# Kernel tuning notes

Hardware: AMD Instinct MI355X
Metric: run time of the kernel (lower is better)

Reference implementation:

```python
import jax, jax.numpy as jnp
import numpy as np

BETA = 0.5
THR = 1.0
BN_EPS = 1e-5

@jax.custom_vjp
def spike(x):
    # heaviside fire: spk = 1[x > 0]
    return (x > 0).astype(x.dtype)

def _spike_fwd(x):
    return spike(x), x

def _spike_bwd(x, g):
    # snnTorch surrogate.atan(), alpha=2: grad = (alpha/2) / (1 + (pi/2*alpha*x)^2) = 1/(1+(pi*x)^2)
    return (g / (1.0 + (jnp.pi * x) ** 2),)

spike.defvjp(_spike_fwd, _spike_bwd)

def setup_inputs() -> dict:
    key = jax.random.key(0)
    ks = jax.random.split(key, 6)
    B, T, D, O = 512, 128, 512, 10
    data = jax.random.normal(ks[0], (B, T, D), dtype=jnp.float32)
    # deterministic Dropout(0.5) mask in {0, 2} (scaled by 1/keep_prob), time-major
    u = jax.random.uniform(ks[1], (T, B, D), dtype=jnp.float32)
    drop_mask = (u > 0.5).astype(jnp.float32) * 2.0
    W1 = jax.random.normal(ks[2], (D, D), dtype=jnp.float32) / np.sqrt(D)
    b1 = jax.random.normal(ks[3], (D,), dtype=jnp.float32) * 0.01
    gamma = jnp.ones((D,), dtype=jnp.float32)
    bn_beta = jnp.zeros((D,), dtype=jnp.float32)
    W2 = jax.random.normal(ks[4], (O, D), dtype=jnp.float32) / np.sqrt(D)
    b2 = jax.random.normal(ks[5], (O,), dtype=jnp.float32) * 0.01
    return {"data": data, "drop_mask": drop_mask, "W1": W1, "b1": b1,
            "gamma": gamma, "bn_beta": bn_beta, "W2": W2, "b2": b2}

def reference(data, drop_mask, W1, b1, gamma, bn_beta, W2, b2):
    B, T, D = data.shape
    O = W2.shape[0]
    xs = jnp.transpose(data, (1, 0, 2))  # [T, B, D] time-major

    def batchnorm(x):  # training-mode BatchNorm1d over batch dim
        mean = jnp.mean(x, axis=0)
        var = jnp.mean((x - mean) ** 2, axis=0)
        return gamma * (x - mean) * jax.lax.rsqrt(var + BN_EPS) + bn_beta

    def step(carry, inp):
        mem1, spk1, mem2, spk2 = carry
        xt, mt = inp
        cur1 = batchnorm((mt * xt) @ W1.T + b1)          # dropout -> linear -> BN
        mem1 = BETA * mem1 + cur1 - spk1 * THR           # Leaky, subtract reset
        spk1 = spike(mem1 - THR)
        cur2 = spk1 @ W2.T + b2
        mem2 = BETA * mem2 + cur2 - spk2 * THR
        spk2 = spike(mem2 - THR)
        return (mem1, spk1, mem2, spk2), spk2

    init = (jnp.zeros((B, D), data.dtype), jnp.zeros((B, D), data.dtype),
            jnp.zeros((B, O), data.dtype), jnp.zeros((B, O), data.dtype))
    _, spk_rec = jax.lax.scan(step, init, (xs, drop_mask))
    return spk_rec  # [T, B, out_size] == torch.stack(spk_rec)
```

## Files before the change

### kernel.cpp

```cpp
#include <hip/hip_runtime.h>
#include <math.h>

#define B_ 512
#define T_ 128
#define D_ 512
#define O_ 10

typedef unsigned int uint32;
typedef short bf16x8 __attribute__((ext_vector_type(8)));
typedef float f32x4 __attribute__((ext_vector_type(4)));

__device__ __forceinline__ uint32 bf16rne(float f) {
    uint32 u = __float_as_uint(f);
    return (u + 0x7FFFu + ((u >> 16) & 1u)) >> 16;
}
__device__ __forceinline__ float bf16f(uint32 h) { return __uint_as_float(h << 16); }

__global__ __launch_bounds__(256)
void presplitW_kernel(const float* __restrict__ W1, unsigned short* __restrict__ Wsp)
{
    const int idx = blockIdx.x * 256 + threadIdx.x;
    const float4 v = *(const float4*)(W1 + (size_t)idx * 4);
    float vv[4] = {v.x, v.y, v.z, v.w};
    uint32 c0[4], c1[4], c2[4];
#pragma unroll
    for (int i = 0; i < 4; ++i) {
        c0[i] = bf16rne(vv[i]);
        float r = vv[i] - bf16f(c0[i]);
        c1[i] = bf16rne(r);
        float r2 = r - bf16f(c1[i]);
        c2[i] = bf16rne(r2);
    }
    const size_t base = (size_t)idx * 4;
    uint2 w;
    w.x = c0[0] | (c0[1] << 16); w.y = c0[2] | (c0[3] << 16);
    *(uint2*)(Wsp + base) = w;
    w.x = c1[0] | (c1[1] << 16); w.y = c1[2] | (c1[3] << 16);
    *(uint2*)(Wsp + 262144 + base) = w;
    w.x = c2[0] | (c2[1] << 16); w.y = c2[2] | (c2[3] << 16);
    *(uint2*)(Wsp + 524288 + base) = w;
}

#define SPW 40
#define SPL (128*SPW)

__global__ __launch_bounds__(256)
void gemm1_kernel(const float* __restrict__ data, const float* __restrict__ drop,
                  const unsigned short* __restrict__ Wsp, const float* __restrict__ b1,
                  float* __restrict__ hbuf, double* __restrict__ pSum,
                  double* __restrict__ pSq, int t0, int Tc)
{
    __shared__ __align__(16) unsigned short As3[3 * SPL];
    __shared__ __align__(16) unsigned short Ws3[3 * SPL];

    const int tid = threadIdx.x;
    const int bid = blockIdx.x;
    const int xcd = bid & 7;
    const int rest = bid >> 3;
    const int yy = rest & 3;
    const int g = (rest >> 2) * 8 + xcd;

    const int R = g * 128;
    const int tc = R >> 9;
    const int b_base = R & 511;
    const int t = t0 + tc;
    const int d0 = yy * 128;

    const int w = tid >> 6;
    const int lane = tid & 63;
    const int wm = w & 1, wn = w >> 1;
    const int q = lane >> 4, r16 = lane & 15;

    f32x4 acc[4][4];
#pragma unroll
    for (int i = 0; i < 4; ++i)
#pragma unroll
        for (int j = 0; j < 4; ++j) acc[i][j] = (f32x4){0.f, 0.f, 0.f, 0.f};

    for (int k0 = 0; k0 < 512; k0 += 32) {
#pragma unroll
        for (int i = 0; i < 2; ++i) {
            const int p = tid + i * 256;
            const int m = p >> 2;
            const int kg = (p & 3) * 8;
            const float* dsrc = data + ((size_t)(b_base + m) * T_ + t) * D_ + k0 + kg;
            const float* msrc = drop + ((size_t)t * B_ + b_base + m) * D_ + k0 + kg;
            const float4 dv0 = *(const float4*)(dsrc);
            const float4 dv1 = *(const float4*)(dsrc + 4);
            const float4 mv0 = *(const float4*)(msrc);
            const float4 mv1 = *(const float4*)(msrc + 4);
            float vv[8] = {dv0.x*mv0.x, dv0.y*mv0.y, dv0.z*mv0.z, dv0.w*mv0.w,
                           dv1.x*mv1.x, dv1.y*mv1.y, dv1.z*mv1.z, dv1.w*mv1.w};
            uint32 u0[8], u1[8], u2[8];
#pragma unroll
            for (int e = 0; e < 8; ++e) {
                u0[e] = bf16rne(vv[e]);
                const float r = vv[e] - bf16f(u0[e]);
                u1[e] = bf16rne(r);
                const float r2 = r - bf16f(u1[e]);
                u2[e] = bf16rne(r2);
            }
            const int dst = m * SPW + kg;
            uint4 pk;
            pk.x = u0[0]|(u0[1]<<16); pk.y = u0[2]|(u0[3]<<16);
            pk.z = u0[4]|(u0[5]<<16); pk.w = u0[6]|(u0[7]<<16);
            *(uint4*)(&As3[dst]) = pk;
            pk.x = u1[0]|(u1[1]<<16); pk.y = u1[2]|(u1[3]<<16);
            pk.z = u1[4]|(u1[5]<<16); pk.w = u1[6]|(u1[7]<<16);
            *(uint4*)(&As3[SPL + dst]) = pk;
            pk.x = u2[0]|(u2[1]<<16); pk.y = u2[2]|(u2[3]<<16);
            pk.z = u2[4]|(u2[5]<<16); pk.w = u2[6]|(u2[7]<<16);
            *(uint4*)(&As3[2*SPL + dst]) = pk;
        }
#pragma unroll
        for (int i = 0; i < 6; ++i) {
            const int p = tid + i * 256;
            const int s = p >> 9;
            const int rem = p & 511;
            const int n = rem >> 2;
            const int kg = (rem & 3) * 8;
            const uint4 pk = *(const uint4*)(Wsp + (size_t)s * 262144
                                             + (size_t)(d0 + n) * 512 + k0 + kg);
            *(uint4*)(&Ws3[s * SPL + n * SPW + kg]) = pk;
        }
        __syncthreads();

        bf16x8 af[4][3], bfr[4][3];
#pragma unroll
        for (int mt = 0; mt < 4; ++mt)
#pragma unroll
            for (int s = 0; s < 3; ++s)
                af[mt][s] = *(const bf16x8*)(&As3[s*SPL + (wm*64 + mt*16 + r16)*SPW + q*8]);
#pragma unroll
        for (int nt = 0; nt < 4; ++nt)
#pragma unroll
            for (int s = 0; s < 3; ++s)
                bfr[nt][s] = *(const bf16x8*)(&Ws3[s*SPL + (wn*64 + nt*16 + r16)*SPW + q*8]);

#define PRODUCT(SA, SB)                                                          \
        {                                                                        \
            _Pragma("unroll")                                                    \
            for (int mt = 0; mt < 4; ++mt) {                                     \
                _Pragma("unroll")                                                \
                for (int nt = 0; nt < 4; ++nt)                                   \
                    acc[mt][nt] = __builtin_amdgcn_mfma_f32_16x16x32_bf16(       \
                        af[mt][SA], bfr[nt][SB], acc[mt][nt], 0, 0, 0);          \
            }                                                                    \
        }
        PRODUCT(0, 0)
        PRODUCT(0, 1)
        PRODUCT(1, 0)
        PRODUCT(1, 1)
        PRODUCT(0, 2)
        PRODUCT(2, 0)
#undef PRODUCT
        __syncthreads();
    }

    float b1c[4];
#pragma unroll
    for (int nt = 0; nt < 4; ++nt) b1c[nt] = b1[d0 + wn*64 + nt*16 + r16];

    double sd[4], sq[4];
#pragma unroll
    for (int nt = 0; nt < 4; ++nt) { sd[nt] = 0.0; sq[nt] = 0.0; }

#pragma unroll
    for (int mt = 0; mt < 4; ++mt)
#pragma unroll
        for (int r = 0; r < 4; ++r) {
            const int row = R + wm*64 + mt*16 + q*4 + r;
            float* op = hbuf + (size_t)row * D_ + d0 + wn*64 + r16;
#pragma unroll
            for (int nt = 0; nt < 4; ++nt) {
                const float hf = acc[mt][nt][r] + b1c[nt];
                op[nt*16] = hf;
                const double dh = (double)hf;
                sd[nt] += dh;
                sq[nt] = fma(dh, dh, sq[nt]);
            }
        }
#pragma unroll
    for (int nt = 0; nt < 4; ++nt) {
        sd[nt] += __shfl_xor(sd[nt], 16); sd[nt] += __shfl_xor(sd[nt], 32);
        sq[nt] += __shfl_xor(sq[nt], 16); sq[nt] += __shfl_xor(sq[nt], 32);
    }
    double* dsh = (double*)&As3[0];
    __syncthreads();
    if (q == 0) {
#pragma unroll
        for (int nt = 0; nt < 4; ++nt) {
            dsh[(w*64 + nt*16 + r16)*2 + 0] = sd[nt];
            dsh[(w*64 + nt*16 + r16)*2 + 1] = sq[nt];
        }
    }
    __syncthreads();
    if (tid < 128) {
        const int col = tid;
        const int gg = col >> 6, c = col & 63;
        const double S = dsh[((2*gg)*64 + c)*2 + 0] + dsh[((2*gg+1)*64 + c)*2 + 0];
        const double Q = dsh[((2*gg)*64 + c)*2 + 1] + dsh[((2*gg+1)*64 + c)*2 + 1];
        const int bt = b_base >> 7;
        pSum[((size_t)(bt*Tc + tc))*D_ + d0 + col] = S;
        pSq [((size_t)(bt*Tc + tc))*D_ + d0 + col] = Q;
    }
}

__global__ __launch_bounds__(256)
void finalize_kernel(const double* __restrict__ pSum, const double* __restrict__ pSq,
                     const float* __restrict__ gamma, const float* __restrict__ bn_beta,
                     float* __restrict__ scaleArr, float* __restrict__ shiftArr, int Tc)
{
    const int tc = blockIdx.x;
    const int d = blockIdx.y * 256 + threadIdx.x;
    double S = 0.0, Q = 0.0;
#pragma unroll
    for (int bt = 0; bt < 4; ++bt) {
        S += pSum[((size_t)(bt * Tc + tc)) * D_ + d];
        Q += pSq [((size_t)(bt * Tc + tc)) * D_ + d];
    }
    const double mean = S / (double)B_;
    const double var  = Q / (double)B_ - mean * mean;
    const double rs   = 1.0 / sqrt(var + 1e-5);
    const double gm   = (double)gamma[d] * rs;
    scaleArr[tc * D_ + d] = (float)gm;
    shiftArr[tc * D_ + d] = (float)((double)bn_beta[d] - gm * mean);
}

__global__ __launch_bounds__(256)
void scanA_kernel(const float* __restrict__ hbuf, const float* __restrict__ scaleArr,
                  const float* __restrict__ shiftArr, unsigned short* __restrict__ spk,
                  float* __restrict__ sMem1, float* __restrict__ sSpk1, int t0, int Tc)
{
    const int idx = blockIdx.x * 256 + threadIdx.x;
    const int b = idx >> 7;
    const int d0 = (idx & 127) * 4;

    float4 m1, s1;
    if (t0 == 0) {
        m1 = make_float4(0.f, 0.f, 0.f, 0.f);
        s1 = make_float4(0.f, 0.f, 0.f, 0.f);
    } else {
        m1 = *(const float4*)(sMem1 + (size_t)b * D_ + d0);
        s1 = *(const float4*)(sSpk1 + (size_t)b * D_ + d0);
    }

    float4 hv = *(const float4*)(hbuf + (size_t)b * D_ + d0);
    float4 sc = *(const float4*)(scaleArr + d0);
    float4 sf = *(const float4*)(shiftArr + d0);

    for (int tc = 0; tc < Tc; ++tc) {
        float4 hvN, scN, sfN;
        if (tc + 1 < Tc) {
            hvN = *(const float4*)(hbuf + ((size_t)(tc + 1) * B_ + b) * D_ + d0);
            scN = *(const float4*)(scaleArr + (tc + 1) * D_ + d0);
            sfN = *(const float4*)(shiftArr + (tc + 1) * D_ + d0);
        }
        float4 cur1;
        cur1.x = fmaf(sc.x, hv.x, sf.x);
        cur1.y = fmaf(sc.y, hv.y, sf.y);
        cur1.z = fmaf(sc.z, hv.z, sf.z);
        cur1.w = fmaf(sc.w, hv.w, sf.w);

        m1.x = fmaf(0.5f, m1.x, cur1.x) - s1.x;
        m1.y = fmaf(0.5f, m1.y, cur1.y) - s1.y;
        m1.z = fmaf(0.5f, m1.z, cur1.z) - s1.z;
        m1.w = fmaf(0.5f, m1.w, cur1.w) - s1.w;

        s1.x = ((m1.x - 1.0f) > 0.f) ? 1.f : 0.f;
        s1.y = ((m1.y - 1.0f) > 0.f) ? 1.f : 0.f;
        s1.z = ((m1.z - 1.0f) > 0.f) ? 1.f : 0.f;
        s1.w = ((m1.w - 1.0f) > 0.f) ? 1.f : 0.f;

        const uint32 ux = (s1.x == 1.f) ? 0x3F80u : 0u;
        const uint32 uy = (s1.y == 1.f) ? 0x3F80u : 0u;
        const uint32 uz = (s1.z == 1.f) ? 0x3F80u : 0u;
        const uint32 uw = (s1.w == 1.f) ? 0x3F80u : 0u;
        uint2 pk;
        pk.x = ux | (uy << 16);
        pk.y = uz | (uw << 16);
        *(uint2*)(spk + ((size_t)tc * B_ + b) * D_ + d0) = pk;

        hv = hvN; sc = scN; sf = sfN;
    }

    *(float4*)(sMem1 + (size_t)b * D_ + d0) = m1;
    *(float4*)(sSpk1 + (size_t)b * D_ + d0) = s1;
}

__global__ __launch_bounds__(256)
void gemm2_kernel(const unsigned short* __restrict__ spk, const float* __restrict__ W2,
                  const float* __restrict__ b2, float* __restrict__ cur2)
{
    const int tid = threadIdx.x;
    const int w = tid >> 6, lane = tid & 63;
    const int rowBase = blockIdx.x * 64 + w * 16;

    float w2r[O_][8];
#pragma unroll
    for (int o = 0; o < O_; ++o) {
        const float4 wa = *(const float4*)(W2 + o * D_ + lane * 8);
        const float4 wb = *(const float4*)(W2 + o * D_ + lane * 8 + 4);
        w2r[o][0] = wa.x; w2r[o][1] = wa.y; w2r[o][2] = wa.z; w2r[o][3] = wa.w;
        w2r[o][4] = wb.x; w2r[o][5] = wb.y; w2r[o][6] = wb.z; w2r[o][7] = wb.w;
    }
    float b2v[O_];
#pragma unroll
    for (int o = 0; o < O_; ++o) b2v[o] = b2[o];

    for (int rr = 0; rr < 16; ++rr) {
        const int row = rowBase + rr;
        const uint4 sv = *(const uint4*)(spk + (size_t)row * D_ + lane * 8);
        float f[8];
        f[0] = bf16f(sv.x & 0xFFFFu); f[1] = bf16f(sv.x >> 16);
        f[2] = bf16f(sv.y & 0xFFFFu); f[3] = bf16f(sv.y >> 16);
        f[4] = bf16f(sv.z & 0xFFFFu); f[5] = bf16f(sv.z >> 16);
        f[6] = bf16f(sv.w & 0xFFFFu); f[7] = bf16f(sv.w >> 16);
        float p[O_];
#pragma unroll
        for (int o = 0; o < O_; ++o) {
            float v = f[0] * w2r[o][0];
#pragma unroll
            for (int j = 1; j < 8; ++j) v = fmaf(f[j], w2r[o][j], v);
            p[o] = v;
        }
#pragma unroll
        for (int o = 0; o < O_; ++o) {
#pragma unroll
            for (int off = 32; off > 0; off >>= 1)
                p[o] += __shfl_xor(p[o], off);
        }
        float outv = 0.f;
#pragma unroll
        for (int o = 0; o < O_; ++o)
            if (lane == o) outv = p[o] + b2v[o];
        if (lane < O_)
            cur2[(size_t)row * O_ + lane] = outv;
    }
}

__global__ __launch_bounds__(256)
void scanB_kernel(const float* __restrict__ cur2, float* __restrict__ out,
                  float* __restrict__ sMem2, float* __restrict__ sSpk2, int t0, int Tc)
{
    const int idx = blockIdx.x * 256 + threadIdx.x;
    float mem2, spk2;
    if (t0 == 0) { mem2 = 0.f; spk2 = 0.f; }
    else { mem2 = sMem2[idx]; spk2 = sSpk2[idx]; }

    float v[4], vn[4];
#pragma unroll
    for (int j = 0; j < 4; ++j) v[j] = cur2[(size_t)j * (B_ * O_) + idx];

    for (int tg = 0; tg < Tc; tg += 4) {
        if (tg + 4 < Tc) {
#pragma unroll
            for (int j = 0; j < 4; ++j)
                vn[j] = cur2[(size_t)(tg + 4 + j) * (B_ * O_) + idx];
        }
#pragma unroll
        for (int j = 0; j < 4; ++j) {
            mem2 = fmaf(0.5f, mem2, v[j]) - spk2;
            spk2 = ((mem2 - 1.0f) > 0.f) ? 1.f : 0.f;
            out[(size_t)(t0 + tg + j) * (B_ * O_) + idx] = spk2;
        }
#pragma unroll
        for (int j = 0; j < 4; ++j) v[j] = vn[j];
    }
    sMem2[idx] = mem2;
    sSpk2[idx] = spk2;
}

extern "C" void kernel_launch(void* const* d_in, const int* in_sizes, int n_in,
                              void* d_out, int out_size, void* d_ws, size_t ws_size,
                              hipStream_t stream) {
    const float* data    = (const float*)d_in[0];
    const float* drop    = (const float*)d_in[1];
    const float* W1      = (const float*)d_in[2];
    const float* b1      = (const float*)d_in[3];
    const float* gamma   = (const float*)d_in[4];
    const float* bn_beta = (const float*)d_in[5];
    const float* W2      = (const float*)d_in[6];
    const float* b2      = (const float*)d_in[7];
    float* out = (float*)d_out;

    const size_t fixedBytes = 1572864  + 2*1048576  + 2*20480 ;
    const size_t perT = 1048576 + 524288 + 20480 + 4096 + 32768;
    int Tc = T_;
    while (Tc > 2 && fixedBytes + (size_t)Tc * perT > ws_size) Tc >>= 1;

    char* p = (char*)d_ws;
    double* pSum    = (double*)p; p += (size_t)4 * Tc * D_ * 8;
    double* pSq     = (double*)p; p += (size_t)4 * Tc * D_ * 8;
    float* hbuf     = (float*)p; p += (size_t)Tc * B_ * D_ * 4;
    float* scaleArr = (float*)p; p += (size_t)Tc * D_ * 4;
    float* shiftArr = (float*)p; p += (size_t)Tc * D_ * 4;
    float* sMem1    = (float*)p; p += (size_t)B_ * D_ * 4;
    float* sSpk1    = (float*)p; p += (size_t)B_ * D_ * 4;
    float* sMem2    = (float*)p; p += (size_t)B_ * O_ * 4;
    float* sSpk2    = (float*)p; p += (size_t)B_ * O_ * 4;
    float* cur2     = (float*)p; p += (size_t)Tc * B_ * O_ * 4;
    unsigned short* Wsp = (unsigned short*)p; p += (size_t)3 * D_ * D_ * 2;
    unsigned short* spk = (unsigned short*)p; p += (size_t)Tc * B_ * D_ * 2;

    presplitW_kernel<<<256, 256, 0, stream>>>(W1, Wsp);

    for (int t0 = 0; t0 < T_; t0 += Tc) {
        gemm1_kernel<<<Tc * 16, 256, 0, stream>>>(data, drop, Wsp, b1, hbuf,
                                                  pSum, pSq, t0, Tc);
        finalize_kernel<<<dim3(Tc, D_ / 256), 256, 0, stream>>>(
            pSum, pSq, gamma, bn_beta, scaleArr, shiftArr, Tc);
        scanA_kernel<<<256, 256, 0, stream>>>(hbuf, scaleArr, shiftArr, spk,
                                              sMem1, sSpk1, t0, Tc);
        gemm2_kernel<<<Tc * 8, 256, 0, stream>>>(spk, W2, b2, cur2);
        scanB_kernel<<<20, 256, 0, stream>>>(cur2, out, sMem2, sSpk2, t0, Tc);
    }
}
```

Baseline: 552.5 us.

## Prefetch GEMM1 operands into registers, repad LDS, widen scanA and gemm2 grids

In gemm1, the next k-tile's data and dropout-mask loads are issued into registers while the current tile's MFMAs run, and the W slices are loaded into registers before the LDS stores. This is meant to hide global-memory latency behind compute. The LDS row pitch shrinks from 40 to 34 halfwords, which changes the bank-conflict pattern and lowers the LDS footprint. scanA now uses one scalar element per thread across 1024 blocks instead of float4 across 256 blocks, and gemm2 uses 4 rows per wave with four times as many blocks, both to expose more parallelism at the cost of narrower memory accesses.

```diff
diff --git a/kernel.cpp b/kernel.cpp
--- a/kernel.cpp
+++ b/kernel.cpp
@@ -41,7 +41,7 @@
     *(uint2*)(Wsp + 524288 + base) = w;
 }
 
-#define SPW 40
+#define SPW 34
 #define SPL (128*SPW)
 
 __global__ __launch_bounds__(256)
@@ -71,26 +71,51 @@
     const int wm = w & 1, wn = w >> 1;
     const int q = lane >> 4, r16 = lane & 15;
 
+    const int lm = tid >> 2;
+    const int kg = (tid & 3) * 8;
+
     f32x4 acc[4][4];
 #pragma unroll
     for (int i = 0; i < 4; ++i)
 #pragma unroll
         for (int j = 0; j < 4; ++j) acc[i][j] = (f32x4){0.f, 0.f, 0.f, 0.f};
 
+    float4 pd[2][2], pm[2][2];
+
+#define LOADA(K0)                                                                \
+    {                                                                            \
+        _Pragma("unroll")                                                        \
+        for (int i = 0; i < 2; ++i) {                                            \
+            const int m = lm + i * 64;                                           \
+            const float* dsrc = data + ((size_t)(b_base + m) * T_ + t) * D_ + (K0) + kg; \
+            const float* msrc = drop + ((size_t)t * B_ + b_base + m) * D_ + (K0) + kg;   \
+            pd[i][0] = *(const float4*)(dsrc);                                   \
+            pd[i][1] = *(const float4*)(dsrc + 4);                               \
+            pm[i][0] = *(const float4*)(msrc);                                   \
+            pm[i][1] = *(const float4*)(msrc + 4);                               \
+        }                                                                        \
+    }
+
+    LOADA(0)
+
     for (int k0 = 0; k0 < 512; k0 += 32) {
+        uint4 pw[6];
+#pragma unroll
+        for (int i = 0; i < 6; ++i) {
+            const int p = tid + i * 256;
+            const int s = p >> 9;
+            const int rem = p & 511;
+            const int n = rem >> 2;
+            const int kg2 = (rem & 3) * 8;
+            pw[i] = *(const uint4*)(Wsp + (size_t)s * 262144
+                                    + (size_t)(d0 + n) * 512 + k0 + kg2);
+        }
 #pragma unroll
         for (int i = 0; i < 2; ++i) {
-            const int p = tid + i * 256;
-            const int m = p >> 2;
-            const int kg = (p & 3) * 8;
-            const float* dsrc = data + ((size_t)(b_base + m) * T_ + t) * D_ + k0 + kg;
-            const float* msrc = drop + ((size_t)t * B_ + b_base + m) * D_ + k0 + kg;
-            const float4 dv0 = *(const float4*)(dsrc);
-            const float4 dv1 = *(const float4*)(dsrc + 4);
-            const float4 mv0 = *(const float4*)(msrc);
-            const float4 mv1 = *(const float4*)(msrc + 4);
-            float vv[8] = {dv0.x*mv0.x, dv0.y*mv0.y, dv0.z*mv0.z, dv0.w*mv0.w,
-                           dv1.x*mv1.x, dv1.y*mv1.y, dv1.z*mv1.z, dv1.w*mv1.w};
+            float vv[8] = {pd[i][0].x*pm[i][0].x, pd[i][0].y*pm[i][0].y,
+                           pd[i][0].z*pm[i][0].z, pd[i][0].w*pm[i][0].w,
+                           pd[i][1].x*pm[i][1].x, pd[i][1].y*pm[i][1].y,
+                           pd[i][1].z*pm[i][1].z, pd[i][1].w*pm[i][1].w};
             uint32 u0[8], u1[8], u2[8];
 #pragma unroll
             for (int e = 0; e < 8; ++e) {
@@ -100,7 +125,7 @@
                 const float r2 = r - bf16f(u1[e]);
                 u2[e] = bf16rne(r2);
             }
-            const int dst = m * SPW + kg;
+            const int dst = (lm + i * 64) * SPW + kg;
             uint4 pk;
             pk.x = u0[0]|(u0[1]<<16); pk.y = u0[2]|(u0[3]<<16);
             pk.z = u0[4]|(u0[5]<<16); pk.w = u0[6]|(u0[7]<<16);
@@ -118,10 +143,8 @@
             const int s = p >> 9;
             const int rem = p & 511;
             const int n = rem >> 2;
-            const int kg = (rem & 3) * 8;
-            const uint4 pk = *(const uint4*)(Wsp + (size_t)s * 262144
-                                             + (size_t)(d0 + n) * 512 + k0 + kg);
-            *(uint4*)(&Ws3[s * SPL + n * SPW + kg]) = pk;
+            const int kg2 = (rem & 3) * 8;
+            *(uint4*)(&Ws3[s * SPL + n * SPW + kg2]) = pw[i];
         }
         __syncthreads();
 
@@ -136,6 +159,8 @@
 #pragma unroll
             for (int s = 0; s < 3; ++s)
                 bfr[nt][s] = *(const bf16x8*)(&Ws3[s*SPL + (wn*64 + nt*16 + r16)*SPW + q*8]);
+
+        if (k0 + 32 < 512) LOADA(k0 + 32)
 
 #define PRODUCT(SA, SB)                                                          \
         {                                                                        \
@@ -232,60 +257,35 @@
                   const float* __restrict__ shiftArr, unsigned short* __restrict__ spk,
                   float* __restrict__ sMem1, float* __restrict__ sSpk1, int t0, int Tc)
 {
-    const int idx = blockIdx.x * 256 + threadIdx.x;
-    const int b = idx >> 7;
-    const int d0 = (idx & 127) * 4;
-
-    float4 m1, s1;
-    if (t0 == 0) {
-        m1 = make_float4(0.f, 0.f, 0.f, 0.f);
-        s1 = make_float4(0.f, 0.f, 0.f, 0.f);
-    } else {
-        m1 = *(const float4*)(sMem1 + (size_t)b * D_ + d0);
-        s1 = *(const float4*)(sSpk1 + (size_t)b * D_ + d0);
-    }
-
-    float4 hv = *(const float4*)(hbuf + (size_t)b * D_ + d0);
-    float4 sc = *(const float4*)(scaleArr + d0);
-    float4 sf = *(const float4*)(shiftArr + d0);
+    const int e = blockIdx.x * 256 + threadIdx.x;
+    const int b = e >> 9;
+    const int d = e & 511;
+
+    float m1, s1;
+    if (t0 == 0) { m1 = 0.f; s1 = 0.f; }
+    else { m1 = sMem1[e]; s1 = sSpk1[e]; }
+
+    float hv = hbuf[e];
+    float sc = scaleArr[d];
+    float sf = shiftArr[d];
 
     for (int tc = 0; tc < Tc; ++tc) {
-        float4 hvN, scN, sfN;
+        float hvN, scN, sfN;
         if (tc + 1 < Tc) {
-            hvN = *(const float4*)(hbuf + ((size_t)(tc + 1) * B_ + b) * D_ + d0);
-            scN = *(const float4*)(scaleArr + (tc + 1) * D_ + d0);
-            sfN = *(const float4*)(shiftArr + (tc + 1) * D_ + d0);
-        }
-        float4 cur1;
-        cur1.x = fmaf(sc.x, hv.x, sf.x);
-        cur1.y = fmaf(sc.y, hv.y, sf.y);
-        cur1.z = fmaf(sc.z, hv.z, sf.z);
-        cur1.w = fmaf(sc.w, hv.w, sf.w);
-
-        m1.x = fmaf(0.5f, m1.x, cur1.x) - s1.x;
-        m1.y = fmaf(0.5f, m1.y, cur1.y) - s1.y;
-        m1.z = fmaf(0.5f, m1.z, cur1.z) - s1.z;
-        m1.w = fmaf(0.5f, m1.w, cur1.w) - s1.w;
-
-        s1.x = ((m1.x - 1.0f) > 0.f) ? 1.f : 0.f;
-        s1.y = ((m1.y - 1.0f) > 0.f) ? 1.f : 0.f;
-        s1.z = ((m1.z - 1.0f) > 0.f) ? 1.f : 0.f;
-        s1.w = ((m1.w - 1.0f) > 0.f) ? 1.f : 0.f;
-
-        const uint32 ux = (s1.x == 1.f) ? 0x3F80u : 0u;
-        const uint32 uy = (s1.y == 1.f) ? 0x3F80u : 0u;
-        const uint32 uz = (s1.z == 1.f) ? 0x3F80u : 0u;
-        const uint32 uw = (s1.w == 1.f) ? 0x3F80u : 0u;
-        uint2 pk;
-        pk.x = ux | (uy << 16);
-        pk.y = uz | (uw << 16);
-        *(uint2*)(spk + ((size_t)tc * B_ + b) * D_ + d0) = pk;
-
+            hvN = hbuf[(size_t)(tc + 1) * (B_ * D_) + e];
+            scN = scaleArr[(tc + 1) * D_ + d];
+            sfN = shiftArr[(tc + 1) * D_ + d];
+        }
+        const float cur1 = fmaf(sc, hv, sf);
+        m1 = fmaf(0.5f, m1, cur1) - s1;
+        s1 = ((m1 - 1.0f) > 0.f) ? 1.f : 0.f;
+        spk[(size_t)tc * (B_ * D_) + e] = (s1 == 1.f) ? (unsigned short)0x3F80u
+                                                      : (unsigned short)0u;
         hv = hvN; sc = scN; sf = sfN;
     }
 
-    *(float4*)(sMem1 + (size_t)b * D_ + d0) = m1;
-    *(float4*)(sSpk1 + (size_t)b * D_ + d0) = s1;
+    sMem1[e] = m1;
+    sSpk1[e] = s1;
 }
 
 __global__ __launch_bounds__(256)
@@ -294,7 +294,7 @@
 {
     const int tid = threadIdx.x;
     const int w = tid >> 6, lane = tid & 63;
-    const int rowBase = blockIdx.x * 64 + w * 16;
+    const int rowBase = blockIdx.x * 16 + w * 4;
 
     float w2r[O_][8];
 #pragma unroll
@@ -308,7 +308,7 @@
 #pragma unroll
     for (int o = 0; o < O_; ++o) b2v[o] = b2[o];
 
-    for (int rr = 0; rr < 16; ++rr) {
+    for (int rr = 0; rr < 4; ++rr) {
         const int row = rowBase + rr;
         const uint4 sv = *(const uint4*)(spk + (size_t)row * D_ + lane * 8);
         float f[8];
@@ -384,7 +384,7 @@
     const float* b2      = (const float*)d_in[7];
     float* out = (float*)d_out;
 
-    const size_t fixedBytes = 1572864  + 2*1048576  + 2*20480 ;
+    const size_t fixedBytes = 1572864 + 2*1048576 + 2*20480;
     const size_t perT = 1048576 + 524288 + 20480 + 4096 + 32768;
     int Tc = T_;
     while (Tc > 2 && fixedBytes + (size_t)Tc * perT > ws_size) Tc >>= 1;
@@ -410,9 +410,9 @@
                                                   pSum, pSq, t0, Tc);
         finalize_kernel<<<dim3(Tc, D_ / 256), 256, 0, stream>>>(
             pSum, pSq, gamma, bn_beta, scaleArr, shiftArr, Tc);
-        scanA_kernel<<<256, 256, 0, stream>>>(hbuf, scaleArr, shiftArr, spk,
-                                              sMem1, sSpk1, t0, Tc);
-        gemm2_kernel<<<Tc * 8, 256, 0, stream>>>(spk, W2, b2, cur2);
+        scanA_kernel<<<(B_ * D_) / 256, 256, 0, stream>>>(hbuf, scaleArr, shiftArr, spk,
+                                                          sMem1, sSpk1, t0, Tc);
+        gemm2_kernel<<<Tc * 32, 256, 0, stream>>>(spk, W2, b2, cur2);
         scanB_kernel<<<20, 256, 0, stream>>>(cur2, out, sMem2, sSpk2, t0, Tc);
     }
 }
```

Result: slower. 622.2 us (+12.6%).
